# Performance work log

Measured on AMD Instinct MI355X. Metric: run time of the kernel, lower is better.

## Reference

```python
import jax, jax.numpy as jnp
import numpy as np

B, C, H, W = 8, 256, 32, 32
DK, HEADS = 64, 4
DQ = DK * HEADS            # lambda attention: query dim = dim_key * num_heads
DV = 256 // HEADS          # out_channels // num_heads
EPS = 1e-5
SF = DK ** (-0.25)


def setup_inputs() -> dict:
    key = jax.random.key(0)
    ks = jax.random.split(key, 6)
    inv = 1.0 / np.sqrt(C)
    return {
        "input": jax.random.normal(ks[0], (B, C, H, W), jnp.float32),
        "Wq": jax.random.normal(ks[1], (DQ, C), jnp.float32) * inv,
        "gamma_q": jnp.ones((DQ,), jnp.float32),
        "beta_q": jnp.zeros((DQ,), jnp.float32),
        "Wk": jax.random.normal(ks[2], (DK, C), jnp.float32) * inv,
        "gamma_k": jnp.ones((DK,), jnp.float32),
        "beta_k": jnp.zeros((DK,), jnp.float32),
        "Wv": jax.random.normal(ks[3], (DV, C), jnp.float32) * inv,
        "rpe": jax.random.normal(ks[4], (2 * max(H, W) - 1, 2 * max(H, W) - 1, DK), jnp.float32),
    }


def _bn(x, gamma, beta):
    # BatchNorm2d in training mode: batch stats over (B, H, W), biased variance
    mu = jnp.mean(x, axis=(0, 2, 3), keepdims=True)
    var = jnp.var(x, axis=(0, 2, 3), keepdims=True)
    xn = (x - mu) * jax.lax.rsqrt(var + EPS)
    return xn * gamma[None, :, None, None] + beta[None, :, None, None]


def reference(input, Wq, gamma_q, beta_q, Wk, gamma_k, beta_k, Wv, rpe):
    b, c, h, w = input.shape
    n = h * w
    size = max(h, w)

    # conv1x1 projections (no bias)
    q = _bn(jnp.einsum('oc,bchw->bohw', Wq, input), gamma_q, beta_q)
    k = _bn(jnp.einsum('oc,bchw->bohw', Wk, input), gamma_k, beta_k)
    v = jnp.einsum('oc,bchw->bohw', Wv, input)

    q = q.reshape(b, HEADS, DK, n) * SF          # [b,h,k,n]
    k = k.reshape(b, DK, n) * SF                 # single kv head -> [b,k,n]
    v = v.reshape(b, DV, n)                      # [b,v,n]

    # lambda attention: content lambda
    ks = jax.nn.softmax(k, axis=-1)
    context = jnp.einsum('bkn,bvn->bkv', ks, v)
    out = jnp.einsum('bkv,bhkn->bhvn', context, q)

    # positional lambda via relative position embedding gather
    pos = jnp.arange(size)
    grid = jnp.stack(jnp.meshgrid(pos, pos, indexing='ij'), axis=-1).reshape(-1, 2)  # [n,2]
    rel = grid[None, :] - grid[:, None] + (size - 1)                                 # [n,n,2]
    rg = rpe[rel[..., 0], rel[..., 1]]                                               # [n,n,k]
    pos_context = jnp.einsum('nmk,bvm->bnkv', rg, v)
    out = out + jnp.einsum('bhkn,bnkv->bhvn', q, pos_context)

    return out.reshape(b, -1, h, w)
```

## Files before the change

kernel.cpp:

```cpp
#include <hip/hip_runtime.h>

#define SFC 0.35355339059327373f

typedef __attribute__((ext_vector_type(8))) short short8;
typedef __attribute__((ext_vector_type(16))) float f32x16;
typedef unsigned short ushort_t;

__device__ __forceinline__ float4 ld4(const float* p) { return *reinterpret_cast<const float4*>(p); }
__device__ __forceinline__ void st4(float* p, float4 v) { *reinterpret_cast<float4*>(p) = v; }

union F4 { float4 v; float f[4]; };
union S8 { short8 v; ushort_t u[8]; };

__device__ __forceinline__ ushort_t bfb(float f) {
  union { float f; unsigned u; } a; a.f = f;
  unsigned r = a.u + 0x7FFFu + ((a.u >> 16) & 1u);
  return (ushort_t)(r >> 16);
}
__device__ __forceinline__ float bf2f(ushort_t u) {
  union { unsigned u; float f; } a; a.u = (unsigned)u << 16; return a.f;
}

__device__ __forceinline__ void gl16(const void* g, void* l) {
  __builtin_amdgcn_global_load_lds(
      (const __attribute__((address_space(1))) unsigned int*)g,
      (__attribute__((address_space(3))) unsigned int*)l, 16, 0, 0);
}

__global__ __launch_bounds__(256) void k_prep(
    const float* __restrict__ rpe, const float* __restrict__ wq,
    const float* __restrict__ wk, const float* __restrict__ wv,
    const float* __restrict__ x, ushort_t* __restrict__ RPEB2,
    ushort_t* __restrict__ WB, ushort_t* __restrict__ XBT)
{
  const int bx = blockIdx.x, t = threadIdx.x;
  if (bx < 63) {
    const int di = bx;
#pragma unroll
    for (int it = 0; it < 2; ++it) {
      const int slot = t + it * 256;
      const int tkc = slot >> 6;
      const int l = slot & 63, lnp = l & 31, hip = l >> 5;
      const int dj = (tkc >> 2) * 32 + lnp;
      const int k = (tkc & 3) * 16 + hip * 8;
      S8 o;
      if (dj < 63) {
        const float* s = rpe + (size_t)di * 4032 + dj * 64 + k;
        float4 a = ld4(s), b = ld4(s + 4);
        o.u[0] = bfb(a.x); o.u[1] = bfb(a.y); o.u[2] = bfb(a.z); o.u[3] = bfb(a.w);
        o.u[4] = bfb(b.x); o.u[5] = bfb(b.y); o.u[6] = bfb(b.z); o.u[7] = bfb(b.w);
      } else {
#pragma unroll
        for (int i = 0; i < 8; ++i) o.u[i] = 0;
      }
      *(short8*)(RPEB2 + (size_t)di * 4096 + tkc * 512 + l * 8) = o.v;
    }
  } else if (bx < 111) {
    const int cc = (bx - 63) * 256 + t;
    const int o = cc >> 5, k8 = (cc & 31) * 8;
    const float* src = (o < 256) ? (wq + o * 256)
                      : (o < 320) ? (wk + (o - 256) * 256)
                                  : (wv + (o - 320) * 256);
    float4 a = ld4(src + k8), b = ld4(src + k8 + 4);
    S8 s;
    s.u[0] = bfb(a.x); s.u[1] = bfb(a.y); s.u[2] = bfb(a.z); s.u[3] = bfb(a.w);
    s.u[4] = bfb(b.x); s.u[5] = bfb(b.y); s.u[6] = bfb(b.z); s.u[7] = bfb(b.w);
    *(short8*)(WB + (size_t)o * 256 + k8) = s.v;
  } else {
    const int id = (bx - 111) * 256 + t;
    const int ng = id & 8191, c8 = id >> 13;
    const int bb = ng >> 10, nn = ng & 1023;
    const float* src = x + (size_t)bb * 262144 + (size_t)(c8 * 8) * 1024 + nn;
    S8 s;
#pragma unroll
    for (int j = 0; j < 8; ++j) s.u[j] = bfb(src[(size_t)j * 1024]);
    *(short8*)(XBT + (size_t)ng * 256 + c8 * 8) = s.v;
  }
}

__global__ __launch_bounds__(256) void k_projm(
    const ushort_t* __restrict__ WB, const ushort_t* __restrict__ XBT,
    float* __restrict__ Pk, ushort_t* __restrict__ QB,
    ushort_t* __restrict__ VB2, float* __restrict__ PSUM,
    float* __restrict__ PSQ)
{
  __shared__ ushort_t SM[13824];
  ushort_t* At = SM;
  ushort_t* Bt = SM + 4608;
  const int t = threadIdx.x;
  const int bm = blockIdx.x, bn = blockIdx.y;
  const int o0 = bm * 64, col0 = bn * 128;
  const int w = t >> 6, l = t & 63, ln = l & 31, hi = l >> 5;
  const int wm = w & 1, wn = w >> 1;

  f32x16 acc0, acc1;
#pragma unroll
  for (int i = 0; i < 16; ++i) { acc0[i] = 0.f; acc1[i] = 0.f; }

  for (int k0 = 0; k0 < 256; k0 += 64) {
    __syncthreads();
#pragma unroll
    for (int i = 0; i < 2; ++i) {
      const int c = t + i * 256, row = c >> 3, k8 = (c & 7) * 8;
      *(short8*)(At + row * 72 + k8) =
          *(const short8*)(WB + (size_t)(o0 + row) * 256 + k0 + k8);
    }
#pragma unroll
    for (int i = 0; i < 4; ++i) {
      const int c = t + i * 256, row = c >> 3, k8 = (c & 7) * 8;
      *(short8*)(Bt + row * 72 + k8) =
          *(const short8*)(XBT + (size_t)(col0 + row) * 256 + k0 + k8);
    }
    __syncthreads();
    const ushort_t* ka  = At + (wm * 32 + ln) * 72 + hi * 8;
    const ushort_t* kb0 = Bt + (wn * 64 + ln) * 72 + hi * 8;
    const ushort_t* kb1 = Bt + (wn * 64 + 32 + ln) * 72 + hi * 8;
#pragma unroll
    for (int kc = 0; kc < 4; ++kc) {
      short8 a = *(const short8*)(ka + kc * 16);
      acc0 = __builtin_amdgcn_mfma_f32_32x32x16_bf16(a, *(const short8*)(kb0 + kc * 16), acc0, 0, 0, 0);
      acc1 = __builtin_amdgcn_mfma_f32_32x32x16_bf16(a, *(const short8*)(kb1 + kc * 16), acc1, 0, 0, 0);
    }
  }

  if (bm == 5) {
    __syncthreads();
    {
      const int n0l = wn * 64 + ln;
#pragma unroll
      for (int r = 0; r < 16; ++r) {
        const int v = wm * 32 + (r & 3) + 8 * (r >> 2) + 4 * hi;
#pragma unroll
        for (int half = 0; half < 2; ++half) {
          const int nl = n0l + half * 32;
          const int i2l = nl >> 5, j2 = nl & 31;
          const float val = half ? acc1[r] : acc0[r];
          SM[((i2l * 4 + wm * 2 + (j2 >> 4)) << 9)
             + ((v & 31) + 32 * ((j2 >> 3) & 1)) * 8 + (j2 & 7)] = bfb(val);
        }
      }
    }
    __syncthreads();
    {
      const int b2 = bn >> 3, i2b0 = (bn & 7) * 4;
      const int slot = t >> 4, off = (t & 15) * 32;
      const int i2l = slot >> 2, sub = slot & 3;
      ushort_t* gdst = VB2 + ((size_t)((b2 * 32 + i2b0 + i2l) * 4 + sub)) * 512 + off;
      const ushort_t* lsrc = SM + slot * 512 + off;
#pragma unroll
      for (int c = 0; c < 4; ++c)
        *(short8*)(gdst + c * 8) = *(const short8*)(lsrc + c * 8);
    }
  } else if (bm == 4) {
#pragma unroll
    for (int r = 0; r < 16; ++r) {
      const int o = o0 + wm * 32 + (r & 3) + 8 * (r >> 2) + 4 * hi;
      float* dst = Pk + (size_t)(o - 256) * 8192 + col0 + wn * 64 + ln;
      dst[0]  = acc0[r];
      dst[32] = acc1[r];
    }
#pragma unroll
    for (int r = 0; r < 16; ++r) {
      float s1 = acc0[r] + acc1[r];
      float s2 = acc0[r] * acc0[r] + acc1[r] * acc1[r];
#pragma unroll
      for (int off = 1; off < 32; off <<= 1) {
        s1 += __shfl_xor(s1, off, 64);
        s2 += __shfl_xor(s2, off, 64);
      }
      if (ln == 0) {
        const int o = o0 + wm * 32 + (r & 3) + 8 * (r >> 2) + 4 * hi;
        PSUM[o * 128 + bn * 2 + wn] = s1;
        PSQ [o * 128 + bn * 2 + wn] = s2;
      }
    }
  } else {
#pragma unroll
    for (int r = 0; r < 16; ++r) {
      float s1 = acc0[r] + acc1[r];
      float s2 = acc0[r] * acc0[r] + acc1[r] * acc1[r];
#pragma unroll
      for (int off = 1; off < 32; off <<= 1) {
        s1 += __shfl_xor(s1, off, 64);
        s2 += __shfl_xor(s2, off, 64);
      }
      if (ln == 0) {
        const int o = o0 + wm * 32 + (r & 3) + 8 * (r >> 2) + 4 * hi;
        PSUM[o * 128 + bn * 2 + wn] = s1;
        PSQ [o * 128 + bn * 2 + wn] = s2;
      }
    }
    __syncthreads();
    {
      const int kcq = 2 * wm;
#pragma unroll
      for (int r = 0; r < 16; ++r) {
        const int kc = kcq + ((r >> 3) & 1);
        const int lq = ln + 32 * ((r >> 2) & 1);
        const int iq = (r & 3) + 4 * hi;
#pragma unroll
        for (int half = 0; half < 2; ++half) {
          const int i1l = wn * 2 + half;
          const float val = half ? acc1[r] : acc0[r];
          SM[((i1l * 4 + kc) << 9) + lq * 8 + iq] = bfb(val);
        }
      }
    }
    __syncthreads();
    {
      const int b0 = col0 >> 10, i1b = (col0 >> 5) & 31;
      const int slot = t >> 4, off = (t & 15) * 32;
      const int i1l = slot >> 2, kc2 = slot & 3;
      ushort_t* gdst = QB + (((size_t)(b0 * 32 + i1b + i1l) * 4 + bm) * 4 + kc2) * 512 + off;
      const ushort_t* lsrc = SM + slot * 512 + off;
#pragma unroll
      for (int c = 0; c < 4; ++c)
        *(short8*)(gdst + c * 8) = *(const short8*)(lsrc + c * 8);
    }
  }
}

__global__ __launch_bounds__(256) void k_softctx(
    const float* __restrict__ Pk, const float* __restrict__ PSUM,
    const float* __restrict__ PSQ, const float* __restrict__ gq,
    const float* __restrict__ bq, const float* __restrict__ gk,
    const float* __restrict__ bk, float* __restrict__ SCALE,
    float* __restrict__ SHIFT, const ushort_t* __restrict__ VB2,
    ushort_t* __restrict__ CTXB)
{
  __shared__ float red[8];
  __shared__ float scsh[2];
  __shared__ float cpart[4][64];
  const int t = threadIdx.x;

  if (blockIdx.x >= 512) {
    const int ch = blockIdx.x - 512;
    float s1 = 0.f, s2 = 0.f;
    if (t < 128) { s1 = PSUM[ch * 128 + t]; s2 = PSQ[ch * 128 + t]; }
#pragma unroll
    for (int off = 1; off < 64; off <<= 1) {
      s1 += __shfl_xor(s1, off, 64);
      s2 += __shfl_xor(s2, off, 64);
    }
    if ((t & 63) == 0) { red[t >> 6] = s1; red[4 + (t >> 6)] = s2; }
    __syncthreads();
    if (t == 0) {
      s1 = red[0] + red[1] + red[2] + red[3];
      s2 = red[4] + red[5] + red[6] + red[7];
      const float mu = s1 * (1.0f / 8192.0f);
      const float var = s2 * (1.0f / 8192.0f) - mu * mu;
      const float sc = rsqrtf(var + 1e-5f) * gq[ch] * SFC;
      SCALE[ch] = sc;
      SHIFT[ch] = bq[ch] * SFC - mu * sc;
    }
    return;
  }

  const int b = blockIdx.x >> 6, kc = blockIdx.x & 63;
  {
    const int ch = 256 + kc;
    float s1 = 0.f, s2 = 0.f;
    if (t < 128) { s1 = PSUM[ch * 128 + t]; s2 = PSQ[ch * 128 + t]; }
#pragma unroll
    for (int off = 1; off < 64; off <<= 1) {
      s1 += __shfl_xor(s1, off, 64);
      s2 += __shfl_xor(s2, off, 64);
    }
    if ((t & 63) == 0) { red[t >> 6] = s1; red[4 + (t >> 6)] = s2; }
    __syncthreads();
    if (t == 0) {
      s1 = red[0] + red[1] + red[2] + red[3];
      s2 = red[4] + red[5] + red[6] + red[7];
      const float mu = s1 * (1.0f / 8192.0f);
      const float var = s2 * (1.0f / 8192.0f) - mu * mu;
      const float sc = rsqrtf(var + 1e-5f) * gk[kc] * SFC;
      scsh[0] = sc;
      scsh[1] = bk[kc] * SFC - mu * sc;
    }
    __syncthreads();
  }
  const float sc = scsh[0], sh = scsh[1];

  const float4* rowp = (const float4*)(Pk + (size_t)kc * 8192 + b * 1024);
  float4 pv = rowp[t];
  float y0 = pv.x * sc + sh, y1 = pv.y * sc + sh;
  float y2 = pv.z * sc + sh, y3 = pv.w * sc + sh;
  float m = fmaxf(fmaxf(y0, y1), fmaxf(y2, y3));
#pragma unroll
  for (int off = 32; off; off >>= 1) m = fmaxf(m, __shfl_xor(m, off, 64));
  __shared__ float red2[8];
  const int w = t >> 6, l = t & 63;
  if (l == 0) red2[w] = m;
  __syncthreads();
  m = fmaxf(fmaxf(red2[0], red2[1]), fmaxf(red2[2], red2[3]));
  const float e0 = __expf(y0 - m), e1 = __expf(y1 - m);
  const float e2 = __expf(y2 - m), e3 = __expf(y3 - m);
  float su = e0 + e1 + e2 + e3;
#pragma unroll
  for (int off = 32; off; off >>= 1) su += __shfl_xor(su, off, 64);
  if (l == 0) red2[4 + w] = su;
  __syncthreads();
  const float inv = 1.0f / (red2[4] + red2[5] + red2[6] + red2[7]);
  const float k0v = e0 * inv, k1v = e1 * inv, k2v = e2 * inv, k3v = e3 * inv;

  const int n0 = t * 4;
  const int i2 = n0 >> 5;
  const int cX = (n0 >> 4) & 1, hi2 = (n0 >> 3) & 1, i0 = n0 & 7;
  const ushort_t* vbL = VB2 + (((size_t)(b * 32 + i2) * 2 + 0) * 2 + cX) * 512
                        + (32 * hi2) * 8 + i0;
  const ushort_t* vbH = vbL + 1024;
  float a64[64];
#pragma unroll
  for (int v = 0; v < 32; ++v) {
    ushort4 u = *(const ushort4*)(vbL + v * 8);
    a64[v] = k0v * bf2f(u.x) + k1v * bf2f(u.y) + k2v * bf2f(u.z) + k3v * bf2f(u.w);
  }
#pragma unroll
  for (int v = 0; v < 32; ++v) {
    ushort4 u = *(const ushort4*)(vbH + v * 8);
    a64[32 + v] = k0v * bf2f(u.x) + k1v * bf2f(u.y) + k2v * bf2f(u.z) + k3v * bf2f(u.w);
  }
  float c32[32];
#pragma unroll
  for (int j = 0; j < 32; ++j) {
    const float mine = (l & 32) ? a64[j + 32] : a64[j];
    const float send = (l & 32) ? a64[j] : a64[j + 32];
    c32[j] = mine + __shfl_xor(send, 32, 64);
  }
  float c16[16];
#pragma unroll
  for (int j = 0; j < 16; ++j) {
    const float mine = (l & 16) ? c32[j + 16] : c32[j];
    const float send = (l & 16) ? c32[j] : c32[j + 16];
    c16[j] = mine + __shfl_xor(send, 16, 64);
  }
  float c8[8];
#pragma unroll
  for (int j = 0; j < 8; ++j) {
    const float mine = (l & 8) ? c16[j + 8] : c16[j];
    const float send = (l & 8) ? c16[j] : c16[j + 8];
    c8[j] = mine + __shfl_xor(send, 8, 64);
  }
  float c4[4];
#pragma unroll
  for (int j = 0; j < 4; ++j) {
    const float mine = (l & 4) ? c8[j + 4] : c8[j];
    const float send = (l & 4) ? c8[j] : c8[j + 4];
    c4[j] = mine + __shfl_xor(send, 4, 64);
  }
  float c2[2];
#pragma unroll
  for (int j = 0; j < 2; ++j) {
    const float mine = (l & 2) ? c4[j + 2] : c4[j];
    const float send = (l & 2) ? c4[j] : c4[j + 2];
    c2[j] = mine + __shfl_xor(send, 2, 64);
  }
  {
    const float mine = (l & 1) ? c2[1] : c2[0];
    const float send = (l & 1) ? c2[0] : c2[1];
    cpart[w][l] = mine + __shfl_xor(send, 1, 64);
  }
  __syncthreads();
  if (w == 0) {
    const float s = cpart[0][l] + cpart[1][l] + cpart[2][l] + cpart[3][l];
    CTXB[(size_t)b * 4608 + l * 72 + kc] = bfb(s);
  }
}

extern __shared__ char ldsc[];

__global__ __launch_bounds__(512, 4) void k_pos(
    const ushort_t* __restrict__ QB, const ushort_t* __restrict__ RPEB2,
    const ushort_t* __restrict__ VB2, const float* __restrict__ SCALE,
    const float* __restrict__ SHIFT, const ushort_t* __restrict__ CTXB,
    float* __restrict__ out)
{
  float* out_l = (float*)ldsc;
  ushort_t* SlB = (ushort_t*)(ldsc + 16896);
  char* CtxL = ldsc + 37376;

  const int t = threadIdx.x;
  const int b = blockIdx.x >> 6;
  const int i1 = (blockIdx.x >> 1) & 31;
  const int hp = blockIdx.x & 1;
  const int w = t >> 6, l = t & 63, ln = l & 31, hi = l >> 5;
  const int h2 = w & 1, g = w >> 1;
  const int m = hp * 2 + h2;

  {
    const char* cs = (const char*)CTXB + (size_t)b * 9216;
    gl16(cs + w * 1024 + l * 16, CtxL + w * 1024 + l * 16);
    if (w == 0) gl16(cs + 8192 + l * 16, CtxL + 8192 + l * 16);
  }

  const ushort_t* rbase = RPEB2 + (size_t)(g * 8 - i1 + 31) * 4096;
  const ushort_t* vbase = VB2 + (size_t)(b * 32 + g * 8) * 2048;

  short8 rA[8];
#pragma unroll
  for (int f = 0; f < 8; ++f) rA[f] = *(const short8*)(rbase + f * 512 + l * 8);

  short8 qf[4];
  {
    const ushort_t* qb = QB + (((size_t)(b * 32 + i1) * 4 + m) * 4) * 512 + l * 8;
#pragma unroll
    for (int kc = 0; kc < 4; ++kc) {
      S8 raw; raw.v = *(const short8*)(qb + kc * 512);
      const int chb = m * 64 + kc * 16 + hi * 8;
      F4 s0, s1, h0, h1;
      s0.v = ld4(SCALE + chb); s1.v = ld4(SCALE + chb + 4);
      h0.v = ld4(SHIFT + chb); h1.v = ld4(SHIFT + chb + 4);
      S8 o;
#pragma unroll
      for (int i = 0; i < 8; ++i) {
        const float f = bf2f(raw.u[i]);
        const float scv = (i < 4) ? s0.f[i] : s1.f[i - 4];
        const float shv = (i < 4) ? h0.f[i] : h1.f[i - 4];
        o.u[i] = bfb(f * scv + shv);
      }
      qf[kc] = o.v;
    }
  }

  f32x16 sv0, sv1;
#pragma unroll
  for (int i = 0; i < 16; ++i) { sv0[i] = 0.f; sv1[i] = 0.f; }

  ushort_t* sm = SlB + w * 1280;

  for (int s = 0; s < 8; ++s) {
    f32x16 t0, t1;
#pragma unroll
    for (int i = 0; i < 16; ++i) { t0[i] = 0.f; t1[i] = 0.f; }
#pragma unroll
    for (int kc = 0; kc < 4; ++kc) {
      t0 = __builtin_amdgcn_mfma_f32_32x32x16_bf16(qf[kc], rA[kc],     t0, 0, 0, 0);
      t1 = __builtin_amdgcn_mfma_f32_32x32x16_bf16(qf[kc], rA[4 + kc], t1, 0, 0, 0);
    }
    if (s + 1 < 8) {
      const ushort_t* rn = rbase + (size_t)(s + 1) * 4096;
#pragma unroll
      for (int f = 0; f < 8; ++f) rA[f] = *(const short8*)(rn + f * 512 + l * 8);
    }
#pragma unroll
    for (int r = 0; r < 16; ++r) {
      const int j1 = (r & 3) + 8 * (r >> 2) + 4 * hi;
      const int j2a = ln + j1 - 31;
      const bool useA = (j2a >= 0);
      const int j2 = useA ? j2a : (j2a + 32);
      sm[j1 * 40 + j2] = bfb(useA ? t0[r] : t1[r]);
    }
    const ushort_t* sa = sm + ln * 40 + hi * 8;
    short8 sA0 = *(const short8*)(sa);
    short8 sA1 = *(const short8*)(sa + 16);
    const ushort_t* vp = vbase + (size_t)s * 2048 + l * 8;
    {
      short8 v00 = *(const short8*)(vp);
      short8 v01 = *(const short8*)(vp + 512);
      sv0 = __builtin_amdgcn_mfma_f32_32x32x16_bf16(sA0, v00, sv0, 0, 0, 0);
      sv0 = __builtin_amdgcn_mfma_f32_32x32x16_bf16(sA1, v01, sv0, 0, 0, 0);
    }
    {
      short8 v10 = *(const short8*)(vp + 1024);
      short8 v11 = *(const short8*)(vp + 1536);
      sv1 = __builtin_amdgcn_mfma_f32_32x32x16_bf16(sA0, v10, sv1, 0, 0, 0);
      sv1 = __builtin_amdgcn_mfma_f32_32x32x16_bf16(sA1, v11, sv1, 0, 0, 0);
    }
  }

  __syncthreads();

  if (g == 0) {
    const ushort_t* cb = (const ushort_t*)CtxL;
    const ushort_t* c0 = cb + ln * 72 + hi * 8;
    const ushort_t* c1 = cb + (32 + ln) * 72 + hi * 8;
#pragma unroll
    for (int kc = 0; kc < 4; ++kc) {
      sv0 = __builtin_amdgcn_mfma_f32_32x32x16_bf16(qf[kc], *(const short8*)(c0 + kc * 16), sv0, 0, 0, 0);
      sv1 = __builtin_amdgcn_mfma_f32_32x32x16_bf16(qf[kc], *(const short8*)(c1 + kc * 16), sv1, 0, 0, 0);
    }
  }

  auto emit = [&](bool add) {
#pragma unroll
    for (int r = 0; r < 16; ++r) {
      const int j1 = (r & 3) + 8 * (r >> 2) + 4 * hi;
      float* p0 = &out_l[(h2 * 64 + ln) * 33 + j1];
      float* p1 = &out_l[(h2 * 64 + 32 + ln) * 33 + j1];
      if (add) { *p0 += sv0[r]; *p1 += sv1[r]; }
      else     { *p0 = sv0[r];  *p1 = sv1[r]; }
    }
  };
  if (g == 3) emit(false);
  __syncthreads();
  if (g == 2) emit(true);
  __syncthreads();
  if (g == 1) emit(true);
  __syncthreads();
  if (g == 0) emit(true);
  __syncthreads();

  {
    const int ch = t >> 2, jh = (t & 3) * 8;
    float* dst = out + (size_t)b * 262144 + (size_t)(hp * 128 + ch) * 1024
                 + i1 * 32 + jh;
    const float* srow = out_l + ch * 33 + jh;
    st4(dst,     make_float4(srow[0], srow[1], srow[2], srow[3]));
    st4(dst + 4, make_float4(srow[4], srow[5], srow[6], srow[7]));
  }
}

extern "C" void kernel_launch(void* const* d_in, const int* in_sizes, int n_in,
                              void* d_out, int out_size, void* d_ws, size_t ws_size,
                              hipStream_t stream) {
  const float* x   = (const float*)d_in[0];
  const float* wq  = (const float*)d_in[1];
  const float* gq  = (const float*)d_in[2];
  const float* bq  = (const float*)d_in[3];
  const float* wk  = (const float*)d_in[4];
  const float* gk  = (const float*)d_in[5];
  const float* bk  = (const float*)d_in[6];
  const float* wv  = (const float*)d_in[7];
  const float* rpe = (const float*)d_in[8];
  float* out = (float*)d_out;
  char* W = (char*)d_ws;

  float* Pk       = (float*)W;
  ushort_t* QB    = (ushort_t*)(W + 2097152);
  float* PSUM     = (float*)(W + 6291456);
  float* PSQ      = (float*)(W + 6455296);
  float* SCALE    = (float*)(W + 6619136);
  float* SHIFT    = (float*)(W + 6621184);
  ushort_t* CTXB  = (ushort_t*)(W + 6623232);
  ushort_t* RPEB2 = (ushort_t*)(W + 6696960);
  ushort_t* VB2   = (ushort_t*)(W + 7213056);
  ushort_t* WB    = (ushort_t*)(W + 8261632);
  ushort_t* XBT   = (ushort_t*)(W + 8458240);

  k_prep<<<1135, 256, 0, stream>>>(rpe, wq, wk, wv, x, RPEB2, WB, XBT);
  k_projm<<<dim3(6, 64), 256, 0, stream>>>(WB, XBT, Pk, QB, VB2, PSUM, PSQ);
  k_softctx<<<768, 256, 0, stream>>>(Pk, PSUM, PSQ, gq, bq, gk, bk,
                                     SCALE, SHIFT, VB2, CTXB);

  hipFuncSetAttribute((const void*)k_pos,
                      hipFuncAttributeMaxDynamicSharedMemorySize, 46592);
  k_pos<<<512, 512, 46592, stream>>>(QB, RPEB2, VB2, SCALE, SHIFT, CTXB, out);
}
```

Before: 56.73 us.

## Fuse weight bf16 conversion into projection GEMM and move RPE prep into softctx

Weight fp32-to-bf16 conversion now happens inline while loading A tiles in the projection kernel, so the separate WB buffer and its prep blocks go away. The RPE bf16 repacking moves from the prep kernel into the 256 spare BN-stats blocks of the softmax/context kernel. The key projection is also stored as bf16 instead of fp32, halving that intermediate's traffic. The cost is that each projection block re-reads and re-converts weights from fp32, and the key path gets a small extra precision loss before softmax.

New measurement: 61.12 us. +7.7%, slower.

```diff
diff --git a/kernel.cpp b/kernel.cpp
--- a/kernel.cpp
+++ b/kernel.cpp
@@ -28,59 +28,22 @@
 }
 
 __global__ __launch_bounds__(256) void k_prep(
-    const float* __restrict__ rpe, const float* __restrict__ wq,
-    const float* __restrict__ wk, const float* __restrict__ wv,
-    const float* __restrict__ x, ushort_t* __restrict__ RPEB2,
-    ushort_t* __restrict__ WB, ushort_t* __restrict__ XBT)
+    const float* __restrict__ x, ushort_t* __restrict__ XBT)
 {
-  const int bx = blockIdx.x, t = threadIdx.x;
-  if (bx < 63) {
-    const int di = bx;
-#pragma unroll
-    for (int it = 0; it < 2; ++it) {
-      const int slot = t + it * 256;
-      const int tkc = slot >> 6;
-      const int l = slot & 63, lnp = l & 31, hip = l >> 5;
-      const int dj = (tkc >> 2) * 32 + lnp;
-      const int k = (tkc & 3) * 16 + hip * 8;
-      S8 o;
-      if (dj < 63) {
-        const float* s = rpe + (size_t)di * 4032 + dj * 64 + k;
-        float4 a = ld4(s), b = ld4(s + 4);
-        o.u[0] = bfb(a.x); o.u[1] = bfb(a.y); o.u[2] = bfb(a.z); o.u[3] = bfb(a.w);
-        o.u[4] = bfb(b.x); o.u[5] = bfb(b.y); o.u[6] = bfb(b.z); o.u[7] = bfb(b.w);
-      } else {
-#pragma unroll
-        for (int i = 0; i < 8; ++i) o.u[i] = 0;
-      }
-      *(short8*)(RPEB2 + (size_t)di * 4096 + tkc * 512 + l * 8) = o.v;
-    }
-  } else if (bx < 111) {
-    const int cc = (bx - 63) * 256 + t;
-    const int o = cc >> 5, k8 = (cc & 31) * 8;
-    const float* src = (o < 256) ? (wq + o * 256)
-                      : (o < 320) ? (wk + (o - 256) * 256)
-                                  : (wv + (o - 320) * 256);
-    float4 a = ld4(src + k8), b = ld4(src + k8 + 4);
-    S8 s;
-    s.u[0] = bfb(a.x); s.u[1] = bfb(a.y); s.u[2] = bfb(a.z); s.u[3] = bfb(a.w);
-    s.u[4] = bfb(b.x); s.u[5] = bfb(b.y); s.u[6] = bfb(b.z); s.u[7] = bfb(b.w);
-    *(short8*)(WB + (size_t)o * 256 + k8) = s.v;
-  } else {
-    const int id = (bx - 111) * 256 + t;
-    const int ng = id & 8191, c8 = id >> 13;
-    const int bb = ng >> 10, nn = ng & 1023;
-    const float* src = x + (size_t)bb * 262144 + (size_t)(c8 * 8) * 1024 + nn;
-    S8 s;
-#pragma unroll
-    for (int j = 0; j < 8; ++j) s.u[j] = bfb(src[(size_t)j * 1024]);
-    *(short8*)(XBT + (size_t)ng * 256 + c8 * 8) = s.v;
-  }
+  const int id = blockIdx.x * 256 + threadIdx.x;
+  const int ng = id & 8191, c8 = id >> 13;
+  const int bb = ng >> 10, nn = ng & 1023;
+  const float* src = x + (size_t)bb * 262144 + (size_t)(c8 * 8) * 1024 + nn;
+  S8 s;
+#pragma unroll
+  for (int j = 0; j < 8; ++j) s.u[j] = bfb(src[(size_t)j * 1024]);
+  *(short8*)(XBT + (size_t)ng * 256 + c8 * 8) = s.v;
 }
 
 __global__ __launch_bounds__(256) void k_projm(
-    const ushort_t* __restrict__ WB, const ushort_t* __restrict__ XBT,
-    float* __restrict__ Pk, ushort_t* __restrict__ QB,
+    const float* __restrict__ wq, const float* __restrict__ wk,
+    const float* __restrict__ wv, const ushort_t* __restrict__ XBT,
+    ushort_t* __restrict__ PkB, ushort_t* __restrict__ QB,
     ushort_t* __restrict__ VB2, float* __restrict__ PSUM,
     float* __restrict__ PSQ)
 {
@@ -93,6 +56,9 @@
   const int w = t >> 6, l = t & 63, ln = l & 31, hi = l >> 5;
   const int wm = w & 1, wn = w >> 1;
 
+  const float* wsrc = (bm < 4) ? (wq + (size_t)o0 * 256)
+                    : (bm == 4) ? wk : wv;
+
   f32x16 acc0, acc1;
 #pragma unroll
   for (int i = 0; i < 16; ++i) { acc0[i] = 0.f; acc1[i] = 0.f; }
@@ -102,8 +68,12 @@
 #pragma unroll
     for (int i = 0; i < 2; ++i) {
       const int c = t + i * 256, row = c >> 3, k8 = (c & 7) * 8;
-      *(short8*)(At + row * 72 + k8) =
-          *(const short8*)(WB + (size_t)(o0 + row) * 256 + k0 + k8);
+      const float* wr = wsrc + (size_t)row * 256 + k0 + k8;
+      float4 a = ld4(wr), b2 = ld4(wr + 4);
+      S8 s;
+      s.u[0] = bfb(a.x); s.u[1] = bfb(a.y); s.u[2] = bfb(a.z); s.u[3] = bfb(a.w);
+      s.u[4] = bfb(b2.x); s.u[5] = bfb(b2.y); s.u[6] = bfb(b2.z); s.u[7] = bfb(b2.w);
+      *(short8*)(At + row * 72 + k8) = s.v;
     }
 #pragma unroll
     for (int i = 0; i < 4; ++i) {
@@ -155,9 +125,9 @@
 #pragma unroll
     for (int r = 0; r < 16; ++r) {
       const int o = o0 + wm * 32 + (r & 3) + 8 * (r >> 2) + 4 * hi;
-      float* dst = Pk + (size_t)(o - 256) * 8192 + col0 + wn * 64 + ln;
-      dst[0]  = acc0[r];
-      dst[32] = acc1[r];
+      ushort_t* dst = PkB + (size_t)(o - 256) * 8192 + col0 + wn * 64 + ln;
+      dst[0]  = bfb(acc0[r]);
+      dst[32] = bfb(acc1[r]);
     }
 #pragma unroll
     for (int r = 0; r < 16; ++r) {
@@ -221,11 +191,12 @@
 }
 
 __global__ __launch_bounds__(256) void k_softctx(
-    const float* __restrict__ Pk, const float* __restrict__ PSUM,
+    const ushort_t* __restrict__ PkB, const float* __restrict__ PSUM,
     const float* __restrict__ PSQ, const float* __restrict__ gq,
     const float* __restrict__ bq, const float* __restrict__ gk,
-    const float* __restrict__ bk, float* __restrict__ SCALE,
-    float* __restrict__ SHIFT, const ushort_t* __restrict__ VB2,
+    const float* __restrict__ bk, const float* __restrict__ rpe,
+    float* __restrict__ SCALE, float* __restrict__ SHIFT,
+    const ushort_t* __restrict__ VB2, ushort_t* __restrict__ RPEB2,
     ushort_t* __restrict__ CTXB)
 {
   __shared__ float red[8];
@@ -234,7 +205,28 @@
   const int t = threadIdx.x;
 
   if (blockIdx.x >= 512) {
-    const int ch = blockIdx.x - 512;
+    const int virt = blockIdx.x - 512;
+    {
+      const int slot = virt * 256 + t;
+      if (slot < 32256) {
+        const int di = slot >> 9, s2 = slot & 511;
+        const int tkc = s2 >> 6, l2 = s2 & 63, lnp = l2 & 31, hip = l2 >> 5;
+        const int dj = (tkc >> 2) * 32 + lnp;
+        const int k = (tkc & 3) * 16 + hip * 8;
+        S8 o;
+        if (dj < 63) {
+          const float* s = rpe + (size_t)di * 4032 + dj * 64 + k;
+          float4 a = ld4(s), b2 = ld4(s + 4);
+          o.u[0] = bfb(a.x); o.u[1] = bfb(a.y); o.u[2] = bfb(a.z); o.u[3] = bfb(a.w);
+          o.u[4] = bfb(b2.x); o.u[5] = bfb(b2.y); o.u[6] = bfb(b2.z); o.u[7] = bfb(b2.w);
+        } else {
+#pragma unroll
+          for (int i = 0; i < 8; ++i) o.u[i] = 0;
+        }
+        *(short8*)(RPEB2 + (size_t)di * 4096 + tkc * 512 + l2 * 8) = o.v;
+      }
+    }
+    const int ch = virt;
     float s1 = 0.f, s2 = 0.f;
     if (t < 128) { s1 = PSUM[ch * 128 + t]; s2 = PSQ[ch * 128 + t]; }
 #pragma unroll
@@ -281,10 +273,10 @@
   }
   const float sc = scsh[0], sh = scsh[1];
 
-  const float4* rowp = (const float4*)(Pk + (size_t)kc * 8192 + b * 1024);
-  float4 pv = rowp[t];
-  float y0 = pv.x * sc + sh, y1 = pv.y * sc + sh;
-  float y2 = pv.z * sc + sh, y3 = pv.w * sc + sh;
+  const ushort4* rowp = (const ushort4*)(PkB + (size_t)kc * 8192 + b * 1024);
+  ushort4 pu = rowp[t];
+  float y0 = bf2f(pu.x) * sc + sh, y1 = bf2f(pu.y) * sc + sh;
+  float y2 = bf2f(pu.z) * sc + sh, y3 = bf2f(pu.w) * sc + sh;
   float m = fmaxf(fmaxf(y0, y1), fmaxf(y2, y3));
 #pragma unroll
   for (int off = 32; off; off >>= 1) m = fmaxf(m, __shfl_xor(m, off, 64));
@@ -525,22 +517,21 @@
   float* out = (float*)d_out;
   char* W = (char*)d_ws;
 
-  float* Pk       = (float*)W;
-  ushort_t* QB    = (ushort_t*)(W + 2097152);
-  float* PSUM     = (float*)(W + 6291456);
-  float* PSQ      = (float*)(W + 6455296);
-  float* SCALE    = (float*)(W + 6619136);
-  float* SHIFT    = (float*)(W + 6621184);
-  ushort_t* CTXB  = (ushort_t*)(W + 6623232);
-  ushort_t* RPEB2 = (ushort_t*)(W + 6696960);
-  ushort_t* VB2   = (ushort_t*)(W + 7213056);
-  ushort_t* WB    = (ushort_t*)(W + 8261632);
-  ushort_t* XBT   = (ushort_t*)(W + 8458240);
-
-  k_prep<<<1135, 256, 0, stream>>>(rpe, wq, wk, wv, x, RPEB2, WB, XBT);
-  k_projm<<<dim3(6, 64), 256, 0, stream>>>(WB, XBT, Pk, QB, VB2, PSUM, PSQ);
-  k_softctx<<<768, 256, 0, stream>>>(Pk, PSUM, PSQ, gq, bq, gk, bk,
-                                     SCALE, SHIFT, VB2, CTXB);
+  ushort_t* PkB   = (ushort_t*)W;
+  ushort_t* QB    = (ushort_t*)(W + 1048576);
+  float* PSUM     = (float*)(W + 5242880);
+  float* PSQ      = (float*)(W + 5406720);
+  float* SCALE    = (float*)(W + 5570560);
+  float* SHIFT    = (float*)(W + 5572608);
+  ushort_t* CTXB  = (ushort_t*)(W + 5574656);
+  ushort_t* RPEB2 = (ushort_t*)(W + 5648384);
+  ushort_t* VB2   = (ushort_t*)(W + 6164480);
+  ushort_t* XBT   = (ushort_t*)(W + 7213056);
+
+  k_prep<<<1024, 256, 0, stream>>>(x, XBT);
+  k_projm<<<dim3(6, 64), 256, 0, stream>>>(wq, wk, wv, XBT, PkB, QB, VB2, PSUM, PSQ);
+  k_softctx<<<768, 256, 0, stream>>>(PkB, PSUM, PSQ, gq, bq, gk, bk, rpe,
+                                     SCALE, SHIFT, VB2, RPEB2, CTXB);
 
   hipFuncSetAttribute((const void*)k_pos,
                       hipFuncAttributeMaxDynamicSharedMemorySize, 46592);
```
